# Kernel tuning notes

Measured on AMD Instinct MI355X. Metric: run time of the kernel, lower is better.

Reference implementation:

```python
import jax, jax.numpy as jnp
import numpy as np

B, T, C, HS = 8, 2048, 1024, 64


def setup_inputs() -> dict:
    key = jax.random.key(0)
    ks = jax.random.split(key, 4)
    x = jax.random.normal(ks[0], (B, T, C), dtype=jnp.float32)
    Wq = jax.random.normal(ks[1], (C, HS), dtype=jnp.float32) * (C ** -0.5)
    Wk = jax.random.normal(ks[2], (C, HS), dtype=jnp.float32) * (C ** -0.5)
    Wv = jax.random.normal(ks[3], (C, HS), dtype=jnp.float32) * (C ** -0.5)
    mask = jnp.tril(jnp.ones((T, T), dtype=jnp.int32))  # causal mask
    return {"x": x, "mask": mask, "Wq": Wq, "Wk": Wk, "Wv": Wv}


def reference(x, mask, Wq, Wk, Wv):
    # x: [B,T,C]; bias-free projections to head_size
    q = jnp.einsum("btc,ch->bth", x, Wq)
    k = jnp.einsum("btc,ch->bth", x, Wk)
    v = jnp.einsum("btc,ch->bth", x, Wv)
    # NOTE: original scales by C**-0.5 (n_embd), not head_size**-0.5
    wei = jnp.einsum("bth,bsh->bts", q, k) * (x.shape[-1] ** -0.5)
    wei = jnp.where(mask[None, :, :] == 0, -jnp.inf, wei)
    wei = jax.nn.softmax(wei, axis=-1)
    # dropout is identity in eval / p=0
    out = jnp.einsum("bts,bsh->bth", wei, v)
    return out
```

## Files before the change

kernel.cpp:

```cpp
#include <hip/hip_runtime.h>
#include <hip/hip_bf16.h>


#define B_  8
#define T_  2048
#define C_  1024
#define HS_ 64
#define MROWS (B_ * T_)

typedef __attribute__((ext_vector_type(8))) short bf16x8;
typedef __attribute__((ext_vector_type(4))) float f32x4;
typedef __attribute__((ext_vector_type(4))) float float4v;

#define SCALE_LOG2 0.04508422037445829f

__device__ __forceinline__ short f2bs(float f) {
    __hip_bfloat16 h = __float2bfloat16(f);
    short s;
    __builtin_memcpy(&s, &h, 2);
    return s;
}

__global__ __launch_bounds__(256) void wt_kernel(
    const float* __restrict__ Wq,
    const float* __restrict__ Wk,
    const float* __restrict__ Wv,
    __hip_bfloat16* __restrict__ Wt) {
    __shared__ float tile[64][65];
    const int m  = blockIdx.x >> 4;
    const int r0 = (blockIdx.x & 15) * 64;
    const float* W = (m == 0) ? Wq : (m == 1) ? Wk : Wv;
    const int i = threadIdx.x >> 6;
    const int j = threadIdx.x & 63;
#pragma unroll
    for (int p = 0; p < 16; ++p) {
        int r = p * 4 + i;
        tile[r][j] = W[(size_t)(r0 + r) * HS_ + j];
    }
    __syncthreads();
#pragma unroll
    for (int p = 0; p < 16; ++p) {
        int h = p * 4 + i;
        Wt[(size_t)m * (HS_ * C_) + (size_t)h * C_ + r0 + j] =
            __float2bfloat16(tile[j][h]);
    }
}

__global__ __launch_bounds__(256, 2) void proj_kernel(
    const float* __restrict__ x,
    const __hip_bfloat16* __restrict__ Wt,
    __hip_bfloat16* __restrict__ Q,
    __hip_bfloat16* __restrict__ Kp,
    __hip_bfloat16* __restrict__ Vt)
{
    __shared__ float xt0[32 * 64];
    __shared__ float xt1[32 * 64];

    const int lane = threadIdx.x & 63;
    const int wave = threadIdx.x >> 6;
    const int quad = lane >> 4;
    const int l15  = lane & 15;
    const int row0 = blockIdx.x * 32;

    const int u16  = lane & 15;
    const int rsub = lane >> 4;
    const float* gsrc[2];
#pragma unroll
    for (int h = 0; h < 2; ++h) {
        int rl = wave * 8 + h * 4 + rsub;
        gsrc[h] = x + (size_t)(row0 + rl) * C_ + ((u16 ^ (rl & 7)) << 2);
    }

    const __hip_bfloat16* wbase[3];
#pragma unroll
    for (int j = 0; j < 3; ++j) {
        int nt = wave * 3 + j;
        int h  = ((nt & 3) * 16) + l15;
        wbase[j] = Wt + (size_t)(nt >> 2) * (HS_ * C_) + (size_t)h * C_ + quad * 8;
    }

    f32x4 acc[2][3];
#pragma unroll
    for (int rt = 0; rt < 2; ++rt)
#pragma unroll
        for (int j = 0; j < 3; ++j)
            acc[rt][j] = (f32x4){0.f, 0.f, 0.f, 0.f};

    bf16x8 bfr0[2][3], bfr1[2][3];

#define ISSUE_DMA(XT, kc)                                                    \
    do {                                                                     \
        _Pragma("unroll")                                                    \
        for (int hh = 0; hh < 2; ++hh)                                       \
            __builtin_amdgcn_global_load_lds(                                \
                (const __attribute__((address_space(1))) unsigned*)          \
                    (gsrc[hh] + (kc)),                                       \
                (__attribute__((address_space(3))) unsigned*)                \
                    (&XT[(wave * 8 + hh * 4) * 64]),                         \
                16, 0, 0);                                                   \
    } while (0)

#define LOAD_B(BF, kc)                                                       \
    do {                                                                     \
        _Pragma("unroll")                                                    \
        for (int ks = 0; ks < 2; ++ks)                                       \
            _Pragma("unroll")                                                \
            for (int j = 0; j < 3; ++j)                                      \
                BF[ks][j] = *(const bf16x8*)(wbase[j] + (kc) + ks * 32);     \
    } while (0)

#define COMPUTE(XT, BF)                                                      \
    do {                                                                     \
        _Pragma("unroll")                                                    \
        for (int ks = 0; ks < 2; ++ks) {                                     \
            bf16x8 a[2];                                                     \
            _Pragma("unroll")                                                \
            for (int rt = 0; rt < 2; ++rt) {                                 \
                const float4v* bp =                                          \
                    (const float4v*)&XT[(rt * 16 + l15) * 64];               \
                const int sw_ = l15 & 7;                                     \
                float4v f0 = bp[(ks * 8 + quad * 2) ^ sw_];                  \
                float4v f1 = bp[(ks * 8 + quad * 2 + 1) ^ sw_];              \
                _Pragma("unroll")                                            \
                for (int e = 0; e < 4; ++e) {                                \
                    a[rt][e]     = f2bs(f0[e]);                              \
                    a[rt][4 + e] = f2bs(f1[e]);                              \
                }                                                            \
            }                                                                \
            _Pragma("unroll")                                                \
            for (int rt = 0; rt < 2; ++rt)                                   \
                _Pragma("unroll")                                            \
                for (int j = 0; j < 3; ++j)                                  \
                    acc[rt][j] = __builtin_amdgcn_mfma_f32_16x16x32_bf16(    \
                        a[rt], BF[ks][j], acc[rt][j], 0, 0, 0);              \
        }                                                                    \
    } while (0)

    ISSUE_DMA(xt0, 0);
    LOAD_B(bfr0, 0);

#pragma unroll 1
    for (int kc = 0; kc < C_; kc += 128) {
        __syncthreads();
        if (kc + 64 < C_) {
            ISSUE_DMA(xt1, kc + 64);
            LOAD_B(bfr1, kc + 64);
        }
        COMPUTE(xt0, bfr0);
        __syncthreads();
        if (kc + 128 < C_) {
            ISSUE_DMA(xt0, kc + 128);
            LOAD_B(bfr0, kc + 128);
        }
        COMPUTE(xt1, bfr1);
    }
#undef ISSUE_DMA
#undef LOAD_B
#undef COMPUTE

#pragma unroll
    for (int rt = 0; rt < 2; ++rt) {
#pragma unroll
        for (int j = 0; j < 3; ++j) {
            int nt  = wave * 3 + j;
            int mtx = nt >> 2;
            int col = (nt & 3) * 16 + l15;
#pragma unroll
            for (int r = 0; r < 4; ++r) {
                int row = row0 + rt * 16 + quad * 4 + r;
                float av = acc[rt][j][r];
                if (mtx == 0) {
                    Q[(size_t)row * HS_ + col] =
                        __float2bfloat16(av * SCALE_LOG2);
                } else if (mtx == 1) {
                    Kp[(size_t)row * HS_ + col] = __float2bfloat16(av);
                } else {
                    int bidx = row >> 11;
                    int t    = row & 2047;
                    Vt[((size_t)bidx * HS_ + col) * T_ + t] =
                        __float2bfloat16(av);
                }
            }
        }
    }
}

__global__ __launch_bounds__(256, 2) void attn_kernel(
    const __hip_bfloat16* __restrict__ Q,
    const __hip_bfloat16* __restrict__ Kp,
    const __hip_bfloat16* __restrict__ Vt,
    float* __restrict__ out)
{
    __shared__ __align__(16) __hip_bfloat16 plds[4][32 * 72];
    __shared__ float o_lds[4][32][65];
    __shared__ float l_lds[4][32];
    __shared__ float l_red[32];

    const int tid  = threadIdx.x;
    const int wv   = tid >> 6;
    const int lane = tid & 63;
    const int quad = lane >> 4;
    const int l15  = lane & 15;
    const int b    = blockIdx.x & 7;
    const int idx  = blockIdx.x >> 3;
    const int lt   = (idx < 32) ? (63 - idx) : (idx - 32);
    const int qb   = lt * 32;
    const int rowg = b * T_ + qb;

    bf16x8 qf[2][2];
#pragma unroll
    for (int rt = 0; rt < 2; ++rt)
#pragma unroll
        for (int h = 0; h < 2; ++h)
            qf[rt][h] = *(const bf16x8*)
                (Q + (size_t)(rowg + rt * 16 + l15) * HS_ + h * 32 + quad * 8);

    f32x4 o[2][4];
#pragma unroll
    for (int rt = 0; rt < 2; ++rt)
#pragma unroll
        for (int j = 0; j < 4; ++j) o[rt][j] = (f32x4){0.f, 0.f, 0.f, 0.f};
    f32x4 ol[2];
    ol[0] = (f32x4){0.f, 0.f, 0.f, 0.f};
    ol[1] = (f32x4){0.f, 0.f, 0.f, 0.f};

    bf16x8 onesf;
#pragma unroll
    for (int e = 0; e < 8; ++e) onesf[e] = (short)0x3F80;

    __hip_bfloat16* pb = plds[wv];
    const int nt = (qb + 31) / 64 + 1;

#define LOADK(KF, kb_)                                                       \
    do {                                                                     \
        const __hip_bfloat16* Kb_ = Kp + (size_t)(b * T_ + (kb_)) * HS_;     \
        _Pragma("unroll")                                                    \
        for (int c = 0; c < 4; ++c)                                          \
            _Pragma("unroll")                                                \
            for (int h = 0; h < 2; ++h)                                      \
                KF[c][h] = *(const bf16x8*)                                  \
                    (Kb_ + (size_t)(c * 16 + l15) * HS_ + h * 32 + quad * 8);\
    } while (0)

#define PROC(KF, kb_)                                                        \
    do {                                                                     \
        bf16x8 vf[2][4];                                                     \
        _Pragma("unroll")                                                    \
        for (int h = 0; h < 2; ++h)                                          \
            _Pragma("unroll")                                                \
            for (int j = 0; j < 4; ++j)                                      \
                vf[h][j] = *(const bf16x8*)                                  \
                    (Vt + ((size_t)b * HS_ + j * 16 + l15) * T_ +            \
                     (kb_) + h * 32 + quad * 8);                             \
        f32x4 s[2][4];                                                       \
        __builtin_amdgcn_s_setprio(1);                                       \
        _Pragma("unroll")                                                    \
        for (int rt = 0; rt < 2; ++rt)                                       \
            _Pragma("unroll")                                                \
            for (int c = 0; c < 4; ++c) {                                    \
                s[rt][c] = (f32x4){0.f, 0.f, 0.f, 0.f};                      \
                s[rt][c] = __builtin_amdgcn_mfma_f32_16x16x32_bf16(          \
                    qf[rt][0], KF[c][0], s[rt][c], 0, 0, 0);                 \
                s[rt][c] = __builtin_amdgcn_mfma_f32_16x16x32_bf16(          \
                    qf[rt][1], KF[c][1], s[rt][c], 0, 0, 0);                 \
            }                                                                \
        __builtin_amdgcn_s_setprio(0);                                       \
        const bool msk = ((kb_) + 63 > qb);                                  \
        _Pragma("unroll")                                                    \
        for (int rt = 0; rt < 2; ++rt)                                       \
            _Pragma("unroll")                                                \
            for (int c = 0; c < 4; ++c)                                      \
                _Pragma("unroll")                                            \
                for (int r = 0; r < 4; ++r) {                                \
                    float pv = __builtin_amdgcn_exp2f(s[rt][c][r]);          \
                    if (msk) {                                               \
                        int row = qb + rt * 16 + quad * 4 + r;               \
                        if ((kb_) + c * 16 + l15 > row) pv = 0.f;            \
                    }                                                        \
                    pb[(rt * 16 + quad * 4 + r) * 72 + c * 16 + l15] =       \
                        __float2bfloat16(pv);                                \
                }                                                            \
        asm volatile("s_waitcnt lgkmcnt(0)" ::: "memory");                   \
        _Pragma("unroll")                                                    \
        for (int rt = 0; rt < 2; ++rt) {                                     \
            bf16x8 pf0 = *(const bf16x8*)                                    \
                (pb + (rt * 16 + l15) * 72 + quad * 8);                      \
            bf16x8 pf1 = *(const bf16x8*)                                    \
                (pb + (rt * 16 + l15) * 72 + 32 + quad * 8);                 \
            __builtin_amdgcn_s_setprio(1);                                   \
            _Pragma("unroll")                                                \
            for (int j = 0; j < 4; ++j) {                                    \
                o[rt][j] = __builtin_amdgcn_mfma_f32_16x16x32_bf16(          \
                    pf0, vf[0][j], o[rt][j], 0, 0, 0);                       \
                o[rt][j] = __builtin_amdgcn_mfma_f32_16x16x32_bf16(          \
                    pf1, vf[1][j], o[rt][j], 0, 0, 0);                       \
            }                                                                \
            ol[rt] = __builtin_amdgcn_mfma_f32_16x16x32_bf16(                \
                pf0, onesf, ol[rt], 0, 0, 0);                                \
            ol[rt] = __builtin_amdgcn_mfma_f32_16x16x32_bf16(                \
                pf1, onesf, ol[rt], 0, 0, 0);                                \
            __builtin_amdgcn_s_setprio(0);                                   \
        }                                                                    \
    } while (0)

    bf16x8 kA[4][2], kB[4][2];
    if (wv < nt) LOADK(kA, wv * 64);
    int i = 0;
#pragma unroll 1
    for (; wv + 4 * (i + 1) < nt; i += 2) {
        LOADK(kB, (wv + 4 * (i + 1)) * 64);
        PROC(kA, (wv + 4 * i) * 64);
        if (wv + 4 * (i + 2) < nt) LOADK(kA, (wv + 4 * (i + 2)) * 64);
        PROC(kB, (wv + 4 * (i + 1)) * 64);
    }
    if (wv + 4 * i < nt) PROC(kA, (wv + 4 * i) * 64);
#undef LOADK
#undef PROC

#pragma unroll
    for (int rt = 0; rt < 2; ++rt)
#pragma unroll
        for (int j = 0; j < 4; ++j)
#pragma unroll
            for (int r = 0; r < 4; ++r)
                o_lds[wv][rt * 16 + quad * 4 + r][j * 16 + l15] = o[rt][j][r];

    if (l15 == 0) {
#pragma unroll
        for (int rt = 0; rt < 2; ++rt)
#pragma unroll
            for (int r = 0; r < 4; ++r)
                l_lds[wv][rt * 16 + quad * 4 + r] = ol[rt][r];
    }
    __syncthreads();

    if (tid < 32) {
        float s = l_lds[0][tid] + l_lds[1][tid] +
                  l_lds[2][tid] + l_lds[3][tid];
        l_red[tid] = 1.0f / s;
    }
    __syncthreads();

    const int h = tid & 63;
#pragma unroll
    for (int k = 0; k < 8; ++k) {
        int row = (tid >> 6) * 8 + k;
        float s = o_lds[0][row][h] + o_lds[1][row][h] +
                  o_lds[2][row][h] + o_lds[3][row][h];
        out[(size_t)(rowg + row) * HS_ + h] = s * l_red[row];
    }
}

extern "C" void kernel_launch(void* const* d_in, const int* in_sizes, int n_in,
                              void* d_out, int out_size, void* d_ws, size_t ws_size,
                              hipStream_t stream) {
    (void)in_sizes; (void)n_in; (void)out_size; (void)ws_size;
    const float* x  = (const float*)d_in[0];
    const float* Wq = (const float*)d_in[2];
    const float* Wk = (const float*)d_in[3];
    const float* Wv = (const float*)d_in[4];

    __hip_bfloat16* ws = (__hip_bfloat16*)d_ws;
    __hip_bfloat16* Wt = ws;
    __hip_bfloat16* Q  = ws + 196608;
    __hip_bfloat16* Kp = ws + 196608 + 1048576;
    __hip_bfloat16* Vt = ws + 196608 + 2 * 1048576;

    wt_kernel<<<48, 256, 0, stream>>>(Wq, Wk, Wv, Wt);
    proj_kernel<<<MROWS / 32, 256, 0, stream>>>(x, Wt, Q, Kp, Vt);
    attn_kernel<<<(T_ / 32) * B_, 256, 0, stream>>>(Q, Kp, Vt, (float*)d_out);
}
```

Baseline: 148.2 us.

## Software-pipeline attention loop across key tiles with double-buffered P in LDS

Splits the per-tile attention work into separate K load, V load, QK matmul, exp/write and PV matmul stages. These are interleaved across consecutive key tiles, so the QK MFMAs of the next tile overlap the exp and LDS traffic of the current one. The P staging buffer in LDS is doubled per wave, and V fragments are now prefetched a tile ahead. The cost is higher register pressure from the extra V and K fragment sets, which could reduce occupancy below the launch-bounds target of 2 blocks.

```diff
diff --git a/kernel.cpp b/kernel.cpp
--- a/kernel.cpp
+++ b/kernel.cpp
@@ -191,7 +191,7 @@
     const __hip_bfloat16* __restrict__ Vt,
     float* __restrict__ out)
 {
-    __shared__ __align__(16) __hip_bfloat16 plds[4][32 * 72];
+    __shared__ __align__(16) __hip_bfloat16 plds[4][2][32 * 72];
     __shared__ float o_lds[4][32][65];
     __shared__ float l_lds[4][32];
     __shared__ float l_red[32];
@@ -228,12 +228,18 @@
 #pragma unroll
     for (int e = 0; e < 8; ++e) onesf[e] = (short)0x3F80;
 
-    __hip_bfloat16* pb = plds[wv];
+    __hip_bfloat16* pb0 = plds[wv][0];
+    __hip_bfloat16* pb1 = plds[wv][1];
     const int nt = (qb + 31) / 64 + 1;
+    const int m  = (wv < nt) ? ((nt - wv + 3) >> 2) : 0;
+    const __hip_bfloat16* Kbase = Kp + (size_t)b * T_ * HS_;
+    const __hip_bfloat16* Vbase = Vt + (size_t)b * HS_ * T_;
+
+#define KB(j) ((wv + 4 * (j)) * 64)
 
 #define LOADK(KF, kb_)                                                       \
     do {                                                                     \
-        const __hip_bfloat16* Kb_ = Kp + (size_t)(b * T_ + (kb_)) * HS_;     \
+        const __hip_bfloat16* Kb_ = Kbase + (size_t)(kb_) * HS_;             \
         _Pragma("unroll")                                                    \
         for (int c = 0; c < 4; ++c)                                          \
             _Pragma("unroll")                                                \
@@ -242,17 +248,19 @@
                     (Kb_ + (size_t)(c * 16 + l15) * HS_ + h * 32 + quad * 8);\
     } while (0)
 
-#define PROC(KF, kb_)                                                        \
-    do {                                                                     \
-        bf16x8 vf[2][4];                                                     \
+#define LOADV(VF, kb_)                                                       \
+    do {                                                                     \
         _Pragma("unroll")                                                    \
         for (int h = 0; h < 2; ++h)                                          \
             _Pragma("unroll")                                                \
             for (int j = 0; j < 4; ++j)                                      \
-                vf[h][j] = *(const bf16x8*)                                  \
-                    (Vt + ((size_t)b * HS_ + j * 16 + l15) * T_ +            \
+                VF[h][j] = *(const bf16x8*)                                  \
+                    (Vbase + (size_t)(j * 16 + l15) * T_ +                   \
                      (kb_) + h * 32 + quad * 8);                             \
-        f32x4 s[2][4];                                                       \
+    } while (0)
+
+#define QKMM(KF)                                                             \
+    do {                                                                     \
         __builtin_amdgcn_s_setprio(1);                                       \
         _Pragma("unroll")                                                    \
         for (int rt = 0; rt < 2; ++rt)                                       \
@@ -265,6 +273,10 @@
                     qf[rt][1], KF[c][1], s[rt][c], 0, 0, 0);                 \
             }                                                                \
         __builtin_amdgcn_s_setprio(0);                                       \
+    } while (0)
+
+#define EXPW(kb_, PB)                                                        \
+    do {                                                                     \
         const bool msk = ((kb_) + 63 > qb);                                  \
         _Pragma("unroll")                                                    \
         for (int rt = 0; rt < 2; ++rt)                                       \
@@ -277,23 +289,27 @@
                         int row = qb + rt * 16 + quad * 4 + r;               \
                         if ((kb_) + c * 16 + l15 > row) pv = 0.f;            \
                     }                                                        \
-                    pb[(rt * 16 + quad * 4 + r) * 72 + c * 16 + l15] =       \
+                    PB[(rt * 16 + quad * 4 + r) * 72 + c * 16 + l15] =       \
                         __float2bfloat16(pv);                                \
                 }                                                            \
+    } while (0)
+
+#define PVMM(PB, VF)                                                         \
+    do {                                                                     \
         asm volatile("s_waitcnt lgkmcnt(0)" ::: "memory");                   \
         _Pragma("unroll")                                                    \
         for (int rt = 0; rt < 2; ++rt) {                                     \
             bf16x8 pf0 = *(const bf16x8*)                                    \
-                (pb + (rt * 16 + l15) * 72 + quad * 8);                      \
+                (PB + (rt * 16 + l15) * 72 + quad * 8);                      \
             bf16x8 pf1 = *(const bf16x8*)                                    \
-                (pb + (rt * 16 + l15) * 72 + 32 + quad * 8);                 \
+                (PB + (rt * 16 + l15) * 72 + 32 + quad * 8);                 \
             __builtin_amdgcn_s_setprio(1);                                   \
             _Pragma("unroll")                                                \
             for (int j = 0; j < 4; ++j) {                                    \
                 o[rt][j] = __builtin_amdgcn_mfma_f32_16x16x32_bf16(          \
-                    pf0, vf[0][j], o[rt][j], 0, 0, 0);                       \
+                    pf0, VF[0][j], o[rt][j], 0, 0, 0);                       \
                 o[rt][j] = __builtin_amdgcn_mfma_f32_16x16x32_bf16(          \
-                    pf1, vf[1][j], o[rt][j], 0, 0, 0);                       \
+                    pf1, VF[1][j], o[rt][j], 0, 0, 0);                       \
             }                                                                \
             ol[rt] = __builtin_amdgcn_mfma_f32_16x16x32_bf16(                \
                 pf0, onesf, ol[rt], 0, 0, 0);                                \
@@ -303,19 +319,44 @@
         }                                                                    \
     } while (0)
 
-    bf16x8 kA[4][2], kB[4][2];
-    if (wv < nt) LOADK(kA, wv * 64);
-    int i = 0;
+    bf16x8 kA[4][2], kB[4][2], vA[2][4], vB[2][4];
+    f32x4 s[2][4];
+
+    if (m > 0) {
+        LOADK(kA, KB(0));
+        LOADV(vA, KB(0));
+        if (m > 1) { LOADK(kB, KB(1)); LOADV(vB, KB(1)); }
+        QKMM(kA);
+        EXPW(KB(0), pb0);
+        int i = 0;
 #pragma unroll 1
-    for (; wv + 4 * (i + 1) < nt; i += 2) {
-        LOADK(kB, (wv + 4 * (i + 1)) * 64);
-        PROC(kA, (wv + 4 * i) * 64);
-        if (wv + 4 * (i + 2) < nt) LOADK(kA, (wv + 4 * (i + 2)) * 64);
-        PROC(kB, (wv + 4 * (i + 1)) * 64);
-    }
-    if (wv + 4 * i < nt) PROC(kA, (wv + 4 * i) * 64);
+        for (; i + 2 < m; i += 2) {
+            QKMM(kB);
+            LOADK(kA, KB(i + 2));
+            PVMM(pb0, vA);
+            EXPW(KB(i + 1), pb1);
+            LOADV(vA, KB(i + 2));
+            QKMM(kA);
+            if (i + 3 < m) LOADK(kB, KB(i + 3));
+            PVMM(pb1, vB);
+            EXPW(KB(i + 2), pb0);
+            if (i + 3 < m) LOADV(vB, KB(i + 3));
+        }
+        if (i + 1 < m) {
+            QKMM(kB);
+            PVMM(pb0, vA);
+            EXPW(KB(i + 1), pb1);
+            PVMM(pb1, vB);
+        } else {
+            PVMM(pb0, vA);
+        }
+    }
 #undef LOADK
-#undef PROC
+#undef LOADV
+#undef QKMM
+#undef EXPW
+#undef PVMM
+#undef KB
 
 #pragma unroll
     for (int rt = 0; rt < 2; ++rt)
@@ -335,9 +376,9 @@
     __syncthreads();
 
     if (tid < 32) {
-        float s = l_lds[0][tid] + l_lds[1][tid] +
-                  l_lds[2][tid] + l_lds[3][tid];
-        l_red[tid] = 1.0f / s;
+        float sum = l_lds[0][tid] + l_lds[1][tid] +
+                    l_lds[2][tid] + l_lds[3][tid];
+        l_red[tid] = 1.0f / sum;
     }
     __syncthreads();
 
@@ -345,9 +386,9 @@
 #pragma unroll
     for (int k = 0; k < 8; ++k) {
         int row = (tid >> 6) * 8 + k;
-        float s = o_lds[0][row][h] + o_lds[1][row][h] +
+        float v = o_lds[0][row][h] + o_lds[1][row][h] +
                   o_lds[2][row][h] + o_lds[3][row][h];
-        out[(size_t)(rowg + row) * HS_ + h] = s * l_red[row];
+        out[(size_t)(rowg + row) * HS_ + h] = v * l_red[row];
     }
 }
 
```

After: 157.5 us. 1.06x slower.
